# Kernel optimization log

Hardware: AMD Instinct MI355X
Metric: run time of the kernel (lower is better)

Reference implementation:

```python
import jax, jax.numpy as jnp
import numpy as np

B, S, H, D = 2, 2048, 16, 64
BLK_Q, BLK_K = 16, 256  # layout row-block = 16 query rows, col-block = 256 key cols


def setup_inputs() -> dict:
    key = jax.random.key(0)
    qkv = jax.random.normal(key, (B, S, 3, H, D), dtype=jnp.float32)
    nq, nk = S // BLK_Q, S // BLK_K  # 128, 8
    layout = np.zeros((nq, nk), dtype=np.int32)
    rows = np.arange(nq)
    layout[rows, (rows * BLK_Q) // BLK_K] = 1  # local diagonal block
    layout[:, 0] = 1                           # global first key block
    return {"qkv": qkv, "layout": jnp.asarray(layout)}


def reference(qkv, layout):
    # qkv: [B, S, 3, H, D], layout: [S//16, S//256] {0,1}
    b, s, _, h, d = qkv.shape
    scale = 1.0 / np.sqrt(d)  # softmax_temp defaults to 1/sqrt(d_keys)
    q = qkv[:, :, 0]  # [B,S,H,D]
    k = qkv[:, :, 1]
    v = qkv[:, :, 2]
    # Expand block layout to a dense [S, S] boolean mask
    mask = jnp.repeat(jnp.repeat(layout.astype(bool), BLK_Q, axis=0), BLK_K, axis=1)[:s, :s]
    scores = jnp.einsum('bshd,bthd->bhst', q, k) * scale  # [B,H,S,S]
    neg_inf = jnp.asarray(-jnp.inf, scores.dtype)
    scores = jnp.where(mask[None, None], scores, neg_inf)
    attn = jax.nn.softmax(scores, axis=-1)  # dropout_p = 0.0 in eval
    out = jnp.einsum('bhst,bthd->bshd', attn, v)  # [B,S,H,D]
    return out
```

## Files before the change

### kernel.cpp

```cpp
#include <hip/hip_runtime.h>

typedef float f32x4 __attribute__((ext_vector_type(4)));
typedef float f32x16 __attribute__((ext_vector_type(16)));
typedef _Float16 f16x8 __attribute__((ext_vector_type(8)));
typedef __fp16 fp16x2 __attribute__((ext_vector_type(2)));
typedef int i32x2 __attribute__((ext_vector_type(2)));

static __device__ __forceinline__ unsigned pk2(float a, float b) {
    fp16x2 r = __builtin_amdgcn_cvt_pkrtz(a, b);
    return __builtin_bit_cast(unsigned, r);
}

#define MFMA32(A, B, C) __builtin_amdgcn_mfma_f32_32x32x16_f16((A), (B), (C), 0, 0, 0)

__global__ __launch_bounds__(128, 2) void fba_fwd(const float* __restrict__ qkv,
                                                  const int* __restrict__ layout,
                                                  float* __restrict__ out) {
    __shared__ unsigned short Klds[2][64 * 64];
    __shared__ unsigned short Vtlds[2][64 * 64];

    const int bid = blockIdx.x;
    const int vid = (bid & 7) * 128 + (bid >> 3);
    const int b = vid >> 9;
    const int hh = (vid >> 5) & 15;
    const int j = (vid >> 2) & 7;
    const int qs = vid & 3;

    const int tid = threadIdx.x;
    const int w = tid >> 6;
    const int lane = tid & 63;
    const int l31 = lane & 31;
    const int h = lane >> 5;

    const size_t bbase = (size_t)b * 2048 * 3072;
    const int qbase = 256 * j + 64 * qs + 32 * w;

    unsigned kbl = 0; int nact = 0;
    for (int kb = 0; kb < 8; ++kb) {
        int a = 0;
        #pragma unroll
        for (int r = 0; r < 4; ++r) a |= layout[(16 * j + 4 * qs + r) * 8 + kb];
        if (a) { kbl |= (unsigned)kb << (4 * nact); ++nact; }
    }
    const int ntile = 4 * nact;

    const float SC = 0.18033688f;
    f16x8 qf[4];
    {
        const float* qp = qkv + bbase + (size_t)(qbase + l31) * 3072 + hh * 64;
        #pragma unroll
        for (int ds = 0; ds < 4; ++ds) {
            const float* p0 = qp + ds * 16 + 8 * h;
            float4 x = *(const float4*)p0;
            float4 y = *(const float4*)(p0 + 4);
            uint4 u;
            u.x = pk2(x.x * SC, x.y * SC); u.y = pk2(x.z * SC, x.w * SC);
            u.z = pk2(y.x * SC, y.y * SC); u.w = pk2(y.z * SC, y.w * SC);
            qf[ds] = __builtin_bit_cast(f16x8, u);
        }
    }

    f32x16 acc[2];
    acc[0] = (f32x16)(0.f);
    acc[1] = (f32x16)(0.f);
    float lsum = 0.f;

    const int skey = tid >> 4;
    const int sdc  = tid & 15;

    float4 kr0, kr1, kr2, kr3, kr4, kr5, kr6, kr7;
    float4 va0, vb0, va1, vb1, va2, vb2, va3, vb3;

#define STAGE_LOAD(ks_) {                                                           \
    const float* kp_ = qkv + bbase + (size_t)((ks_) + skey) * 3072 + 1024 + hh * 64 + sdc * 4; \
    kr0 = *(const float4*)kp_;                                                      \
    kr1 = *(const float4*)(kp_ +  8 * 3072);                                        \
    kr2 = *(const float4*)(kp_ + 16 * 3072);                                        \
    kr3 = *(const float4*)(kp_ + 24 * 3072);                                        \
    kr4 = *(const float4*)(kp_ + 32 * 3072);                                        \
    kr5 = *(const float4*)(kp_ + 40 * 3072);                                        \
    kr6 = *(const float4*)(kp_ + 48 * 3072);                                        \
    kr7 = *(const float4*)(kp_ + 56 * 3072);                                        \
    const float* vp_ = qkv + bbase + (size_t)((ks_) + 2 * skey) * 3072 + 2048 + hh * 64 + sdc * 4; \
    va0 = *(const float4*)vp_;              vb0 = *(const float4*)(vp_ +      3072); \
    va1 = *(const float4*)(vp_ + 16 * 3072); vb1 = *(const float4*)(vp_ + 17 * 3072); \
    va2 = *(const float4*)(vp_ + 32 * 3072); vb2 = *(const float4*)(vp_ + 33 * 3072); \
    va3 = *(const float4*)(vp_ + 48 * 3072); vb3 = *(const float4*)(vp_ + 49 * 3072); \
}

#define WK(m, krm) *(uint2*)((char*)KB + ((((skey + 8 * (m)) * 128 + sdc * 8)) ^ (skey << 4))) = \
    make_uint2(pk2(krm.x, krm.y), pk2(krm.z, krm.w));
#define WV(m, vam, vbm) {                                                           \
    const float* a_ = &vam.x; const float* b_ = &vbm.x;                             \
    _Pragma("unroll")                                                               \
    for (int e2 = 0; e2 < 4; ++e2) {                                                \
        int d_ = 4 * sdc + e2;                                                      \
        int off_ = (d_ * 128 + (2 * skey + 16 * (m)) * 2) ^ (((d_ ^ (d_ >> 3)) & 7) << 4); \
        *(unsigned*)((char*)VB + off_) = pk2(a_[e2], b_[e2]);                       \
    }                                                                               \
}
#define STAGE_WRITE(nb) {                                                           \
    unsigned short* KB = &Klds[nb][0];                                              \
    WK(0, kr0) WK(1, kr1) WK(2, kr2) WK(3, kr3)                                     \
    WK(4, kr4) WK(5, kr5) WK(6, kr6) WK(7, kr7)                                     \
    unsigned short* VB = &Vtlds[nb][0];                                             \
    WV(0, va0, vb0) WV(1, va1, vb1) WV(2, va2, vb2) WV(3, va3, vb3)                 \
}

    {
        int kb0 = kbl & 15;
        STAGE_LOAD(kb0 * 256);
        STAGE_WRITE(0);
    }
    __syncthreads();

    for (int t = 0; t < ntile; ++t) {
        const bool more = (t + 1 < ntile);
        if (more) {
            int t2 = t + 1;
            int kb = (kbl >> (4 * (t2 >> 2))) & 15;
            STAGE_LOAD(kb * 256 + (t2 & 3) * 64);
        }
        {
            const int cur = t & 1;
            const unsigned short* KB = &Klds[cur][0];
            const unsigned short* VB = &Vtlds[cur][0];
            #pragma unroll
            for (int kt = 0; kt < 2; ++kt) {
                const int key = kt * 32 + l31;
                const int kswz = (l31 & 7) << 4;
                f16x8 kf[4];
                #pragma unroll
                for (int ds = 0; ds < 4; ++ds)
                    kf[ds] = *(const f16x8*)((const char*)KB + ((key * 128 + ds * 32 + h * 16) ^ kswz));
                f16x8 vf[2][2];
                #pragma unroll
                for (int dt = 0; dt < 2; ++dt) {
                    const int d = dt * 32 + l31;
                    const int vswz = ((d ^ (d >> 3)) & 7) << 4;
                    #pragma unroll
                    for (int ks = 0; ks < 2; ++ks)
                        vf[dt][ks] = *(const f16x8*)((const char*)VB + ((d * 128 + kt * 64 + ks * 32 + h * 16) ^ vswz));
                }
                f32x16 st = (f32x16)(0.f);
                st = MFMA32(kf[0], qf[0], st);
                st = MFMA32(kf[1], qf[1], st);
                st = MFMA32(kf[2], qf[2], st);
                st = MFMA32(kf[3], qf[3], st);
                unsigned ulo[4], uhi[4];
                float psum = 0.f;
                #pragma unroll
                for (int jq = 0; jq < 4; ++jq) {
                    float a0 = exp2f(st[4 * jq + 0]);
                    float a1 = exp2f(st[4 * jq + 1]);
                    float a2 = exp2f(st[4 * jq + 2]);
                    float a3 = exp2f(st[4 * jq + 3]);
                    psum += (a0 + a1) + (a2 + a3);
                    ulo[jq] = pk2(a0, a1);
                    uhi[jq] = pk2(a2, a3);
                }
                lsum += psum;
                #pragma unroll
                for (int ks = 0; ks < 2; ++ks) {
                    i32x2 r0 = __builtin_amdgcn_permlane32_swap((int)ulo[2 * ks], (int)ulo[2 * ks + 1], false, false);
                    i32x2 r1 = __builtin_amdgcn_permlane32_swap((int)uhi[2 * ks], (int)uhi[2 * ks + 1], false, false);
                    uint4 uw;
                    uw.x = (unsigned)r0[0]; uw.y = (unsigned)r1[0];
                    uw.z = (unsigned)r0[1]; uw.w = (unsigned)r1[1];
                    f16x8 pf = __builtin_bit_cast(f16x8, uw);
                    acc[0] = MFMA32(vf[0][ks], pf, acc[0]);
                    acc[1] = MFMA32(vf[1][ks], pf, acc[1]);
                }
            }
        }
        if (more) STAGE_WRITE((t + 1) & 1);
        __syncthreads();
    }

    lsum += __shfl_xor(lsum, 32);
    const float inv = 1.0f / lsum;
    float* op = out + (((size_t)b * 2048 + (qbase + l31)) * 16 + hh) * 64;
    #pragma unroll
    for (int dt = 0; dt < 2; ++dt)
        #pragma unroll
        for (int jq = 0; jq < 4; ++jq) {
            float4 o;
            o.x = acc[dt][4 * jq + 0] * inv;
            o.y = acc[dt][4 * jq + 1] * inv;
            o.z = acc[dt][4 * jq + 2] * inv;
            o.w = acc[dt][4 * jq + 3] * inv;
            *(float4*)(op + dt * 32 + 8 * jq + 4 * h) = o;
        }
}

extern "C" void kernel_launch(void* const* d_in, const int* in_sizes, int n_in,
                              void* d_out, int out_size, void* d_ws, size_t ws_size,
                              hipStream_t stream) {
    const float* qkv = (const float*)d_in[0];
    const int* layout = (const int*)d_in[1];
    float* out = (float*)d_out;
    fba_fwd<<<dim3(1024), dim3(128), 0, stream>>>(qkv, layout, out);
}
```

Before: 29.82 us.

## Split key tile across two extra waves per block with LDS reduction

Doubles the block to 256 threads, giving four waves. Each pair of waves shares a 32-row query slice and takes one half of each 64-key tile. Staging loads are spread across more threads, so each thread holds fewer prefetch registers. At the end, the second wave of each pair writes its partial accumulators and row sum to LDS, and the first wave adds them and normalizes the output. This aims to raise parallelism and latency hiding per block, at the cost of an extra barrier and an LDS reduction. Q fragments are now loaded redundantly by both waves of a pair.

New measurement: 49.25 us. 65.1% more time.

```diff
diff --git a/kernel.cpp b/kernel.cpp
--- a/kernel.cpp
+++ b/kernel.cpp
@@ -13,7 +13,7 @@
 
 #define MFMA32(A, B, C) __builtin_amdgcn_mfma_f32_32x32x16_f16((A), (B), (C), 0, 0, 0)
 
-__global__ __launch_bounds__(128, 2) void fba_fwd(const float* __restrict__ qkv,
+__global__ __launch_bounds__(256, 4) void fba_fwd(const float* __restrict__ qkv,
                                                   const int* __restrict__ layout,
                                                   float* __restrict__ out) {
     __shared__ unsigned short Klds[2][64 * 64];
@@ -28,12 +28,14 @@
 
     const int tid = threadIdx.x;
     const int w = tid >> 6;
+    const int qw = w >> 1;
+    const int ks = w & 1;
     const int lane = tid & 63;
     const int l31 = lane & 31;
     const int h = lane >> 5;
 
     const size_t bbase = (size_t)b * 2048 * 3072;
-    const int qbase = 256 * j + 64 * qs + 32 * w;
+    const int qbase = 256 * j + 64 * qs + 32 * qw;
 
     unsigned kbl = 0; int nact = 0;
     for (int kb = 0; kb < 8; ++kb) {
@@ -68,43 +70,36 @@
     const int skey = tid >> 4;
     const int sdc  = tid & 15;
 
-    float4 kr0, kr1, kr2, kr3, kr4, kr5, kr6, kr7;
-    float4 va0, vb0, va1, vb1, va2, vb2, va3, vb3;
+    float4 kr0, kr1, kr2, kr3;
+    float4 va0, vb0, va1, vb1;
 
 #define STAGE_LOAD(ks_) {                                                           \
     const float* kp_ = qkv + bbase + (size_t)((ks_) + skey) * 3072 + 1024 + hh * 64 + sdc * 4; \
     kr0 = *(const float4*)kp_;                                                      \
-    kr1 = *(const float4*)(kp_ +  8 * 3072);                                        \
-    kr2 = *(const float4*)(kp_ + 16 * 3072);                                        \
-    kr3 = *(const float4*)(kp_ + 24 * 3072);                                        \
-    kr4 = *(const float4*)(kp_ + 32 * 3072);                                        \
-    kr5 = *(const float4*)(kp_ + 40 * 3072);                                        \
-    kr6 = *(const float4*)(kp_ + 48 * 3072);                                        \
-    kr7 = *(const float4*)(kp_ + 56 * 3072);                                        \
+    kr1 = *(const float4*)(kp_ + 16 * 3072);                                        \
+    kr2 = *(const float4*)(kp_ + 32 * 3072);                                        \
+    kr3 = *(const float4*)(kp_ + 48 * 3072);                                        \
     const float* vp_ = qkv + bbase + (size_t)((ks_) + 2 * skey) * 3072 + 2048 + hh * 64 + sdc * 4; \
-    va0 = *(const float4*)vp_;              vb0 = *(const float4*)(vp_ +      3072); \
-    va1 = *(const float4*)(vp_ + 16 * 3072); vb1 = *(const float4*)(vp_ + 17 * 3072); \
-    va2 = *(const float4*)(vp_ + 32 * 3072); vb2 = *(const float4*)(vp_ + 33 * 3072); \
-    va3 = *(const float4*)(vp_ + 48 * 3072); vb3 = *(const float4*)(vp_ + 49 * 3072); \
-}
-
-#define WK(m, krm) *(uint2*)((char*)KB + ((((skey + 8 * (m)) * 128 + sdc * 8)) ^ (skey << 4))) = \
+    va0 = *(const float4*)vp_;               vb0 = *(const float4*)(vp_ +      3072); \
+    va1 = *(const float4*)(vp_ + 32 * 3072); vb1 = *(const float4*)(vp_ + 33 * 3072); \
+}
+
+#define WK(m, krm) *(uint2*)((char*)KB + ((((skey + 16 * (m)) * 128 + sdc * 8)) ^ ((skey & 7) << 4))) = \
     make_uint2(pk2(krm.x, krm.y), pk2(krm.z, krm.w));
 #define WV(m, vam, vbm) {                                                           \
     const float* a_ = &vam.x; const float* b_ = &vbm.x;                             \
     _Pragma("unroll")                                                               \
     for (int e2 = 0; e2 < 4; ++e2) {                                                \
         int d_ = 4 * sdc + e2;                                                      \
-        int off_ = (d_ * 128 + (2 * skey + 16 * (m)) * 2) ^ (((d_ ^ (d_ >> 3)) & 7) << 4); \
+        int off_ = (d_ * 128 + (2 * skey + 32 * (m)) * 2) ^ (((d_ ^ (d_ >> 3)) & 7) << 4); \
         *(unsigned*)((char*)VB + off_) = pk2(a_[e2], b_[e2]);                       \
     }                                                                               \
 }
 #define STAGE_WRITE(nb) {                                                           \
     unsigned short* KB = &Klds[nb][0];                                              \
     WK(0, kr0) WK(1, kr1) WK(2, kr2) WK(3, kr3)                                     \
-    WK(4, kr4) WK(5, kr5) WK(6, kr6) WK(7, kr7)                                     \
     unsigned short* VB = &Vtlds[nb][0];                                             \
-    WV(0, va0, vb0) WV(1, va1, vb1) WV(2, va2, vb2) WV(3, va3, vb3)                 \
+    WV(0, va0, vb0) WV(1, va1, vb1)                                                 \
 }
 
     {
@@ -125,52 +120,49 @@
             const int cur = t & 1;
             const unsigned short* KB = &Klds[cur][0];
             const unsigned short* VB = &Vtlds[cur][0];
-            #pragma unroll
-            for (int kt = 0; kt < 2; ++kt) {
-                const int key = kt * 32 + l31;
-                const int kswz = (l31 & 7) << 4;
-                f16x8 kf[4];
+            const int key = ks * 32 + l31;
+            const int kswz = (l31 & 7) << 4;
+            f16x8 kf[4];
+            #pragma unroll
+            for (int ds = 0; ds < 4; ++ds)
+                kf[ds] = *(const f16x8*)((const char*)KB + ((key * 128 + ds * 32 + h * 16) ^ kswz));
+            f16x8 vf[2][2];
+            #pragma unroll
+            for (int dt = 0; dt < 2; ++dt) {
+                const int d = dt * 32 + l31;
+                const int vswz = ((d ^ (d >> 3)) & 7) << 4;
                 #pragma unroll
-                for (int ds = 0; ds < 4; ++ds)
-                    kf[ds] = *(const f16x8*)((const char*)KB + ((key * 128 + ds * 32 + h * 16) ^ kswz));
-                f16x8 vf[2][2];
-                #pragma unroll
-                for (int dt = 0; dt < 2; ++dt) {
-                    const int d = dt * 32 + l31;
-                    const int vswz = ((d ^ (d >> 3)) & 7) << 4;
-                    #pragma unroll
-                    for (int ks = 0; ks < 2; ++ks)
-                        vf[dt][ks] = *(const f16x8*)((const char*)VB + ((d * 128 + kt * 64 + ks * 32 + h * 16) ^ vswz));
-                }
-                f32x16 st = (f32x16)(0.f);
-                st = MFMA32(kf[0], qf[0], st);
-                st = MFMA32(kf[1], qf[1], st);
-                st = MFMA32(kf[2], qf[2], st);
-                st = MFMA32(kf[3], qf[3], st);
-                unsigned ulo[4], uhi[4];
-                float psum = 0.f;
-                #pragma unroll
-                for (int jq = 0; jq < 4; ++jq) {
-                    float a0 = exp2f(st[4 * jq + 0]);
-                    float a1 = exp2f(st[4 * jq + 1]);
-                    float a2 = exp2f(st[4 * jq + 2]);
-                    float a3 = exp2f(st[4 * jq + 3]);
-                    psum += (a0 + a1) + (a2 + a3);
-                    ulo[jq] = pk2(a0, a1);
-                    uhi[jq] = pk2(a2, a3);
-                }
-                lsum += psum;
-                #pragma unroll
-                for (int ks = 0; ks < 2; ++ks) {
-                    i32x2 r0 = __builtin_amdgcn_permlane32_swap((int)ulo[2 * ks], (int)ulo[2 * ks + 1], false, false);
-                    i32x2 r1 = __builtin_amdgcn_permlane32_swap((int)uhi[2 * ks], (int)uhi[2 * ks + 1], false, false);
-                    uint4 uw;
-                    uw.x = (unsigned)r0[0]; uw.y = (unsigned)r1[0];
-                    uw.z = (unsigned)r0[1]; uw.w = (unsigned)r1[1];
-                    f16x8 pf = __builtin_bit_cast(f16x8, uw);
-                    acc[0] = MFMA32(vf[0][ks], pf, acc[0]);
-                    acc[1] = MFMA32(vf[1][ks], pf, acc[1]);
-                }
+                for (int ksi = 0; ksi < 2; ++ksi)
+                    vf[dt][ksi] = *(const f16x8*)((const char*)VB + ((d * 128 + ks * 64 + ksi * 32 + h * 16) ^ vswz));
+            }
+            f32x16 st = (f32x16)(0.f);
+            st = MFMA32(kf[0], qf[0], st);
+            st = MFMA32(kf[1], qf[1], st);
+            st = MFMA32(kf[2], qf[2], st);
+            st = MFMA32(kf[3], qf[3], st);
+            unsigned ulo[4], uhi[4];
+            float psum = 0.f;
+            #pragma unroll
+            for (int jq = 0; jq < 4; ++jq) {
+                float a0 = exp2f(st[4 * jq + 0]);
+                float a1 = exp2f(st[4 * jq + 1]);
+                float a2 = exp2f(st[4 * jq + 2]);
+                float a3 = exp2f(st[4 * jq + 3]);
+                psum += (a0 + a1) + (a2 + a3);
+                ulo[jq] = pk2(a0, a1);
+                uhi[jq] = pk2(a2, a3);
+            }
+            lsum += psum;
+            #pragma unroll
+            for (int ksi = 0; ksi < 2; ++ksi) {
+                i32x2 r0 = __builtin_amdgcn_permlane32_swap((int)ulo[2 * ksi], (int)ulo[2 * ksi + 1], false, false);
+                i32x2 r1 = __builtin_amdgcn_permlane32_swap((int)uhi[2 * ksi], (int)uhi[2 * ksi + 1], false, false);
+                uint4 uw;
+                uw.x = (unsigned)r0[0]; uw.y = (unsigned)r1[0];
+                uw.z = (unsigned)r0[1]; uw.w = (unsigned)r1[1];
+                f16x8 pf = __builtin_bit_cast(f16x8, uw);
+                acc[0] = MFMA32(vf[0][ksi], pf, acc[0]);
+                acc[1] = MFMA32(vf[1][ksi], pf, acc[1]);
             }
         }
         if (more) STAGE_WRITE((t + 1) & 1);
@@ -178,19 +170,37 @@
     }
 
     lsum += __shfl_xor(lsum, 32);
-    const float inv = 1.0f / lsum;
-    float* op = out + (((size_t)b * 2048 + (qbase + l31)) * 16 + hh) * 64;
-    #pragma unroll
-    for (int dt = 0; dt < 2; ++dt)
-        #pragma unroll
-        for (int jq = 0; jq < 4; ++jq) {
-            float4 o;
-            o.x = acc[dt][4 * jq + 0] * inv;
-            o.y = acc[dt][4 * jq + 1] * inv;
-            o.z = acc[dt][4 * jq + 2] * inv;
-            o.w = acc[dt][4 * jq + 3] * inv;
-            *(float4*)(op + dt * 32 + 8 * jq + 4 * h) = o;
-        }
+    float* sh = (qw == 0) ? (float*)&Klds[0][0] : (float*)&Vtlds[0][0];
+    if (ks == 1) {
+        float* p = sh + lane * 34;
+        #pragma unroll
+        for (int i = 0; i < 16; ++i) p[i] = acc[0][i];
+        #pragma unroll
+        for (int i = 0; i < 16; ++i) p[16 + i] = acc[1][i];
+        p[32] = lsum;
+    }
+    __syncthreads();
+    if (ks == 0) {
+        const float* p = sh + lane * 34;
+        #pragma unroll
+        for (int i = 0; i < 16; ++i) acc[0][i] += p[i];
+        #pragma unroll
+        for (int i = 0; i < 16; ++i) acc[1][i] += p[16 + i];
+        lsum += p[32];
+        const float inv = 1.0f / lsum;
+        float* op = out + (((size_t)b * 2048 + (qbase + l31)) * 16 + hh) * 64;
+        #pragma unroll
+        for (int dt = 0; dt < 2; ++dt)
+            #pragma unroll
+            for (int jq = 0; jq < 4; ++jq) {
+                float4 o;
+                o.x = acc[dt][4 * jq + 0] * inv;
+                o.y = acc[dt][4 * jq + 1] * inv;
+                o.z = acc[dt][4 * jq + 2] * inv;
+                o.w = acc[dt][4 * jq + 3] * inv;
+                *(float4*)(op + dt * 32 + 8 * jq + 4 * h) = o;
+            }
+    }
 }
 
 extern "C" void kernel_launch(void* const* d_in, const int* in_sizes, int n_in,
@@ -199,5 +209,5 @@
     const float* qkv = (const float*)d_in[0];
     const int* layout = (const int*)d_in[1];
     float* out = (float*)d_out;
-    fba_fwd<<<dim3(1024), dim3(128), 0, stream>>>(qkv, layout, out);
-}
+    fba_fwd<<<dim3(1024), dim3(256), 0, stream>>>(qkv, layout, out);
+}
```

## Deepen K/V prefetch to two register sets and add MFMA priority hints

Applied to the files above, without the earlier changes.

Keeps two register sets of K/V global loads in flight, each issued two tiles ahead, and unrolls the main loop by two so each set alternates between the two LDS buffers. It also marks the key block list wave-uniform with readfirstlane, raises wave priority around the MFMA groups, and staggers the key half each wave processes first (kt ^ w) so the two waves read different LDS rows. The goal is to hide global-load latency and reduce LDS bank contention, at the cost of holding 16 more float4 registers, which may lower occupancy or cause spills.

Result: slower. 83.82 us (+181.1%).

```diff
diff --git a/kernel.cpp b/kernel.cpp
--- a/kernel.cpp
+++ b/kernel.cpp
@@ -42,6 +42,7 @@
         for (int r = 0; r < 4; ++r) a |= layout[(16 * j + 4 * qs + r) * 8 + kb];
         if (a) { kbl |= (unsigned)kb << (4 * nact); ++nact; }
     }
+    kbl = __builtin_amdgcn_readfirstlane(kbl);
     const int ntile = 4 * nact;
 
     const float SC = 0.18033688f;
@@ -68,112 +69,114 @@
     const int skey = tid >> 4;
     const int sdc  = tid & 15;
 
-    float4 kr0, kr1, kr2, kr3, kr4, kr5, kr6, kr7;
-    float4 va0, vb0, va1, vb1, va2, vb2, va3, vb3;
-
-#define STAGE_LOAD(ks_) {                                                           \
+#define DECL_SET(S) float4 k0##S, k1##S, k2##S, k3##S, k4##S, k5##S, k6##S, k7##S, \
+                           a0##S, b0##S, a1##S, b1##S, a2##S, b2##S, a3##S, b3##S;
+    DECL_SET(A)
+    DECL_SET(B)
+
+#define STAGE_LOAD(S, ks_) {                                                        \
     const float* kp_ = qkv + bbase + (size_t)((ks_) + skey) * 3072 + 1024 + hh * 64 + sdc * 4; \
-    kr0 = *(const float4*)kp_;                                                      \
-    kr1 = *(const float4*)(kp_ +  8 * 3072);                                        \
-    kr2 = *(const float4*)(kp_ + 16 * 3072);                                        \
-    kr3 = *(const float4*)(kp_ + 24 * 3072);                                        \
-    kr4 = *(const float4*)(kp_ + 32 * 3072);                                        \
-    kr5 = *(const float4*)(kp_ + 40 * 3072);                                        \
-    kr6 = *(const float4*)(kp_ + 48 * 3072);                                        \
-    kr7 = *(const float4*)(kp_ + 56 * 3072);                                        \
+    k0##S = *(const float4*)kp_;                                                    \
+    k1##S = *(const float4*)(kp_ +  8 * 3072);                                      \
+    k2##S = *(const float4*)(kp_ + 16 * 3072);                                      \
+    k3##S = *(const float4*)(kp_ + 24 * 3072);                                      \
+    k4##S = *(const float4*)(kp_ + 32 * 3072);                                      \
+    k5##S = *(const float4*)(kp_ + 40 * 3072);                                      \
+    k6##S = *(const float4*)(kp_ + 48 * 3072);                                      \
+    k7##S = *(const float4*)(kp_ + 56 * 3072);                                      \
     const float* vp_ = qkv + bbase + (size_t)((ks_) + 2 * skey) * 3072 + 2048 + hh * 64 + sdc * 4; \
-    va0 = *(const float4*)vp_;              vb0 = *(const float4*)(vp_ +      3072); \
-    va1 = *(const float4*)(vp_ + 16 * 3072); vb1 = *(const float4*)(vp_ + 17 * 3072); \
-    va2 = *(const float4*)(vp_ + 32 * 3072); vb2 = *(const float4*)(vp_ + 33 * 3072); \
-    va3 = *(const float4*)(vp_ + 48 * 3072); vb3 = *(const float4*)(vp_ + 49 * 3072); \
-}
-
-#define WK(m, krm) *(uint2*)((char*)KB + ((((skey + 8 * (m)) * 128 + sdc * 8)) ^ (skey << 4))) = \
-    make_uint2(pk2(krm.x, krm.y), pk2(krm.z, krm.w));
-#define WV(m, vam, vbm) {                                                           \
-    const float* a_ = &vam.x; const float* b_ = &vbm.x;                             \
+    a0##S = *(const float4*)vp_;               b0##S = *(const float4*)(vp_ +      3072); \
+    a1##S = *(const float4*)(vp_ + 16 * 3072); b1##S = *(const float4*)(vp_ + 17 * 3072); \
+    a2##S = *(const float4*)(vp_ + 32 * 3072); b2##S = *(const float4*)(vp_ + 33 * 3072); \
+    a3##S = *(const float4*)(vp_ + 48 * 3072); b3##S = *(const float4*)(vp_ + 49 * 3072); \
+}
+
+#define WK1(S, m, KB) *(uint2*)((char*)(KB) + ((((skey + 8 * (m)) * 128 + sdc * 8)) ^ (skey << 4))) = \
+    make_uint2(pk2(k##m##S.x, k##m##S.y), pk2(k##m##S.z, k##m##S.w));
+#define WV1(S, p, VB) {                                                             \
+    const float* A_ = &a##p##S.x; const float* B_ = &b##p##S.x;                     \
     _Pragma("unroll")                                                               \
     for (int e2 = 0; e2 < 4; ++e2) {                                                \
         int d_ = 4 * sdc + e2;                                                      \
-        int off_ = (d_ * 128 + (2 * skey + 16 * (m)) * 2) ^ (((d_ ^ (d_ >> 3)) & 7) << 4); \
-        *(unsigned*)((char*)VB + off_) = pk2(a_[e2], b_[e2]);                       \
+        int off_ = (d_ * 128 + (2 * skey + 16 * (p)) * 2) ^ (((d_ ^ (d_ >> 3)) & 7) << 4); \
+        *(unsigned*)((char*)(VB) + off_) = pk2(A_[e2], B_[e2]);                     \
     }                                                                               \
 }
-#define STAGE_WRITE(nb) {                                                           \
+#define STAGE_WRITE(S, nb) {                                                        \
     unsigned short* KB = &Klds[nb][0];                                              \
-    WK(0, kr0) WK(1, kr1) WK(2, kr2) WK(3, kr3)                                     \
-    WK(4, kr4) WK(5, kr5) WK(6, kr6) WK(7, kr7)                                     \
+    WK1(S, 0, KB) WK1(S, 1, KB) WK1(S, 2, KB) WK1(S, 3, KB)                         \
+    WK1(S, 4, KB) WK1(S, 5, KB) WK1(S, 6, KB) WK1(S, 7, KB)                         \
     unsigned short* VB = &Vtlds[nb][0];                                             \
-    WV(0, va0, vb0) WV(1, va1, vb1) WV(2, va2, vb2) WV(3, va3, vb3)                 \
-}
-
-    {
-        int kb0 = kbl & 15;
-        STAGE_LOAD(kb0 * 256);
-        STAGE_WRITE(0);
-    }
+    WV1(S, 0, VB) WV1(S, 1, VB) WV1(S, 2, VB) WV1(S, 3, VB)                         \
+}
+
+#define COMPUTE(KB, VB) {                                                           \
+    _Pragma("unroll")                                                               \
+    for (int kti = 0; kti < 2; ++kti) {                                             \
+        const int kt = kti ^ w;                     \
+        const int key = kt * 32 + l31;                                              \
+        const int kswz = (l31 & 7) << 4;                                            \
+        f16x8 kf[4];                                                                \
+        _Pragma("unroll")                                                           \
+        for (int ds = 0; ds < 4; ++ds)                                              \
+            kf[ds] = *(const f16x8*)((const char*)(KB) + ((key * 128 + ds * 32 + h * 16) ^ kswz)); \
+        f16x8 vf[2][2];                                                             \
+        _Pragma("unroll")                                                           \
+        for (int dt = 0; dt < 2; ++dt) {                                            \
+            const int d = dt * 32 + l31;                                            \
+            const int vswz = ((d ^ (d >> 3)) & 7) << 4;                             \
+            _Pragma("unroll")                                                       \
+            for (int ksi = 0; ksi < 2; ++ksi)                                       \
+                vf[dt][ksi] = *(const f16x8*)((const char*)(VB) + ((d * 128 + kt * 64 + ksi * 32 + h * 16) ^ vswz)); \
+        }                                                                           \
+        __builtin_amdgcn_s_setprio(1);                                              \
+        f32x16 st = (f32x16)(0.f);                                                  \
+        st = MFMA32(kf[0], qf[0], st);                                              \
+        st = MFMA32(kf[1], qf[1], st);                                              \
+        st = MFMA32(kf[2], qf[2], st);                                              \
+        st = MFMA32(kf[3], qf[3], st);                                              \
+        __builtin_amdgcn_s_setprio(0);                                              \
+        unsigned ulo[4], uhi[4];                                                    \
+        float psum = 0.f;                                                           \
+        _Pragma("unroll")                                                           \
+        for (int jq = 0; jq < 4; ++jq) {                                            \
+            float e0 = exp2f(st[4 * jq + 0]), e1 = exp2f(st[4 * jq + 1]);           \
+            float e2 = exp2f(st[4 * jq + 2]), e3 = exp2f(st[4 * jq + 3]);           \
+            psum += (e0 + e1) + (e2 + e3);                                          \
+            ulo[jq] = pk2(e0, e1); uhi[jq] = pk2(e2, e3);                           \
+        }                                                                           \
+        lsum += psum;                                                               \
+        __builtin_amdgcn_s_setprio(1);                                              \
+        _Pragma("unroll")                                                           \
+        for (int ksi = 0; ksi < 2; ++ksi) {                                         \
+            i32x2 r0 = __builtin_amdgcn_permlane32_swap((int)ulo[2 * ksi], (int)ulo[2 * ksi + 1], false, false); \
+            i32x2 r1 = __builtin_amdgcn_permlane32_swap((int)uhi[2 * ksi], (int)uhi[2 * ksi + 1], false, false); \
+            uint4 uw;                                                               \
+            uw.x = (unsigned)r0[0]; uw.y = (unsigned)r1[0];                         \
+            uw.z = (unsigned)r0[1]; uw.w = (unsigned)r1[1];                         \
+            f16x8 pf = __builtin_bit_cast(f16x8, uw);                               \
+            acc[0] = MFMA32(vf[0][ksi], pf, acc[0]);                                \
+            acc[1] = MFMA32(vf[1][ksi], pf, acc[1]);                                \
+        }                                                                           \
+        __builtin_amdgcn_s_setprio(0);                                              \
+    }                                                                               \
+}
+
+#define TB(t_) ((int)(((kbl >> (((t_) >> 2) * 4)) & 15) * 256 + ((t_) & 3) * 64))
+
+    STAGE_LOAD(A, TB(0));
+    STAGE_LOAD(B, TB(1));
+    STAGE_WRITE(A, 0);
     __syncthreads();
 
-    for (int t = 0; t < ntile; ++t) {
-        const bool more = (t + 1 < ntile);
-        if (more) {
-            int t2 = t + 1;
-            int kb = (kbl >> (4 * (t2 >> 2))) & 15;
-            STAGE_LOAD(kb * 256 + (t2 & 3) * 64);
-        }
-        {
-            const int cur = t & 1;
-            const unsigned short* KB = &Klds[cur][0];
-            const unsigned short* VB = &Vtlds[cur][0];
-            #pragma unroll
-            for (int kt = 0; kt < 2; ++kt) {
-                const int key = kt * 32 + l31;
-                const int kswz = (l31 & 7) << 4;
-                f16x8 kf[4];
-                #pragma unroll
-                for (int ds = 0; ds < 4; ++ds)
-                    kf[ds] = *(const f16x8*)((const char*)KB + ((key * 128 + ds * 32 + h * 16) ^ kswz));
-                f16x8 vf[2][2];
-                #pragma unroll
-                for (int dt = 0; dt < 2; ++dt) {
-                    const int d = dt * 32 + l31;
-                    const int vswz = ((d ^ (d >> 3)) & 7) << 4;
-                    #pragma unroll
-                    for (int ks = 0; ks < 2; ++ks)
-                        vf[dt][ks] = *(const f16x8*)((const char*)VB + ((d * 128 + kt * 64 + ks * 32 + h * 16) ^ vswz));
-                }
-                f32x16 st = (f32x16)(0.f);
-                st = MFMA32(kf[0], qf[0], st);
-                st = MFMA32(kf[1], qf[1], st);
-                st = MFMA32(kf[2], qf[2], st);
-                st = MFMA32(kf[3], qf[3], st);
-                unsigned ulo[4], uhi[4];
-                float psum = 0.f;
-                #pragma unroll
-                for (int jq = 0; jq < 4; ++jq) {
-                    float a0 = exp2f(st[4 * jq + 0]);
-                    float a1 = exp2f(st[4 * jq + 1]);
-                    float a2 = exp2f(st[4 * jq + 2]);
-                    float a3 = exp2f(st[4 * jq + 3]);
-                    psum += (a0 + a1) + (a2 + a3);
-                    ulo[jq] = pk2(a0, a1);
-                    uhi[jq] = pk2(a2, a3);
-                }
-                lsum += psum;
-                #pragma unroll
-                for (int ks = 0; ks < 2; ++ks) {
-                    i32x2 r0 = __builtin_amdgcn_permlane32_swap((int)ulo[2 * ks], (int)ulo[2 * ks + 1], false, false);
-                    i32x2 r1 = __builtin_amdgcn_permlane32_swap((int)uhi[2 * ks], (int)uhi[2 * ks + 1], false, false);
-                    uint4 uw;
-                    uw.x = (unsigned)r0[0]; uw.y = (unsigned)r1[0];
-                    uw.z = (unsigned)r0[1]; uw.w = (unsigned)r1[1];
-                    f16x8 pf = __builtin_bit_cast(f16x8, uw);
-                    acc[0] = MFMA32(vf[0][ks], pf, acc[0]);
-                    acc[1] = MFMA32(vf[1][ks], pf, acc[1]);
-                }
-            }
-        }
-        if (more) STAGE_WRITE((t + 1) & 1);
+    for (int t = 0; t < ntile; t += 2) {
+        if (t + 2 < ntile) STAGE_LOAD(A, TB(t + 2));
+        COMPUTE(&Klds[0][0], &Vtlds[0][0]);
+        STAGE_WRITE(B, 1);
+        __syncthreads();
+        if (t + 3 < ntile) STAGE_LOAD(B, TB(t + 3));
+        COMPUTE(&Klds[1][0], &Vtlds[1][0]);
+        if (t + 2 < ntile) STAGE_WRITE(A, 0);
         __syncthreads();
     }
 
```
